# Kernel optimization log

Measured on AMD Instinct MI355X. Metric: run time of the kernel, lower is better.

Reference implementation:

```python
import jax, jax.numpy as jnp
import numpy as np

B, T, I, H, C = 16384, 1024, 1, 2, 4  # batch, seq_len, input_size, hidden_size, num_classes


def setup_inputs() -> dict:
    key = jax.random.key(0)
    ks = jax.random.split(key, 7)
    s = 1.0 / np.sqrt(H).astype(np.float32)  # PyTorch default init range
    u = lambda k, shape: jax.random.uniform(k, shape, dtype=jnp.float32, minval=-s, maxval=s)
    return {
        "x": jax.random.normal(ks[0], (B, T, I), dtype=jnp.float32),
        "W_ih": u(ks[1], (4 * H, I)),   # gate order: i, f, g, o (PyTorch convention)
        "W_hh": u(ks[2], (4 * H, H)),
        "b_ih": u(ks[3], (4 * H,)),
        "b_hh": u(ks[4], (4 * H,)),
        "W_fc": u(ks[5], (C, H)),
        "b_fc": u(ks[6], (C,)),
    }


def _lstm_last_hidden(x, W_ih, W_hh, b_ih, b_hh):
    # Precompute the input contribution for all timesteps: [B, T, 4H]
    x_proj = jnp.einsum('bti,gi->btg', x, W_ih) + (b_ih + b_hh)
    h0 = jnp.zeros((x.shape[0], H), dtype=x.dtype)
    c0 = jnp.zeros((x.shape[0], H), dtype=x.dtype)

    def step(carry, xp_t):
        h, c = carry
        gates = xp_t + h @ W_hh.T              # [B, 4H]
        i, f, g, o = jnp.split(gates, 4, axis=-1)
        c = jax.nn.sigmoid(f) * c + jax.nn.sigmoid(i) * jnp.tanh(g)
        h = jax.nn.sigmoid(o) * jnp.tanh(c)
        return (h, c), None

    (h_last, _), _ = jax.lax.scan(step, (h0, c0), jnp.swapaxes(x_proj, 0, 1))
    return h_last  # [B, H]


def reference(x, W_ih, W_hh, b_ih, b_hh, W_fc, b_fc):
    h_last = _lstm_last_hidden(x, W_ih, W_hh, b_ih, b_hh)
    return h_last @ W_fc.T + b_fc  # [B, C]
```

## Files before the change

kernel.cpp:

```cpp
#include <hip/hip_runtime.h>


typedef float f32x2 __attribute__((ext_vector_type(2)));

static __device__ __forceinline__ float fast_exp2(float x) { return __builtin_amdgcn_exp2f(x); }
static __device__ __forceinline__ float fast_rcp(float x)  { return __builtin_amdgcn_rcpf(x); }

static __device__ __forceinline__ float dpp_swap1(float v) {
    int i = __builtin_bit_cast(int, v);
    i = __builtin_amdgcn_mov_dpp(i, 0xB1, 0xF, 0xF, false);
    return __builtin_bit_cast(float, i);
}

#define SIG_SCALE  (-1.4426950408889634f)
#define TANH_SCALE ( 2.8853900817779268f)

__global__ __launch_bounds__(64, 1) void lstm_fused3(
    const float* __restrict__ x,
    const float* __restrict__ W_ih,
    const float* __restrict__ W_hh,
    const float* __restrict__ b_ih,
    const float* __restrict__ b_hh,
    const float* __restrict__ W_fc,
    const float* __restrict__ b_fc,
    float* __restrict__ out,
    int T)
{
    const int tid = blockIdx.x * 64 + threadIdx.x;
    const int e   = tid >> 1;
    const int j   = tid & 1;

    float wihs[4], whm[4], whp[4], bbs[4];
#pragma unroll
    for (int k = 0; k < 4; ++k) {
        const int g = 2 * k + j;
        const float s = (k == 2) ? TANH_SCALE : SIG_SCALE;
        wihs[k] = s * W_ih[g];
        whm[k]  = s * W_hh[2 * g + j];
        whp[k]  = s * W_hh[2 * g + (j ^ 1)];
        bbs[k]  = s * (b_ih[g] + b_hh[g]);
    }

    f32x2 wihs2[2], whm2[2], whp2[2], bbs2[2];
#pragma unroll
    for (int q = 0; q < 2; ++q) {
        wihs2[q] = f32x2{wihs[2*q], wihs[2*q+1]};
        whm2[q]  = f32x2{whm[2*q],  whm[2*q+1]};
        whp2[q]  = f32x2{whp[2*q],  whp[2*q+1]};
        bbs2[q]  = f32x2{bbs[2*q],  bbs[2*q+1]};
    }

    float hm = 0.f;
    float hp = 0.f;
    float c  = 0.f;

    const float4* xv = reinterpret_cast<const float4*>(x + (size_t)e * (size_t)T);
    const int nt4 = T >> 2;

    for (int t4 = 0; t4 < nt4; ++t4) {
        const float4 xq = xv[t4];
        const float xs[4] = {xq.x, xq.y, xq.z, xq.w};

        f32x2 xterm[4][2];
#pragma unroll
        for (int u = 0; u < 4; ++u) {
            const f32x2 xu = f32x2{xs[u], xs[u]};
#pragma unroll
            for (int q = 0; q < 2; ++q)
                xterm[u][q] = __builtin_elementwise_fma(xu, wihs2[q], bbs2[q]);
        }

#pragma unroll
        for (int u = 0; u < 4; ++u) {
            const f32x2 hmv = f32x2{hm, hm};
            const f32x2 hpv = f32x2{hp, hp};
            const f32x2 pre01 = __builtin_elementwise_fma(
                whm2[0], hmv, __builtin_elementwise_fma(whp2[0], hpv, xterm[u][0]));
            const f32x2 pre23 = __builtin_elementwise_fma(
                whm2[1], hmv, __builtin_elementwise_fma(whp2[1], hpv, xterm[u][1]));

            const float Eg = fast_exp2(pre23.x);
            const float Ef = fast_exp2(pre01.y);
            const float Ei = fast_exp2(pre01.x);
            const float Eo = fast_exp2(pre23.y);

            const float F   = 1.f + Ef;
            const float Gp  = 1.f + Eg;
            const float Ip  = 1.f + Ei;
            const float Oo  = 1.f + Eo;

            const float GmF = fmaf(Eg, F, -F);
            const float cp  = c * Ip;
            const float B   = (F * Ip) * Gp;
            const float A   = fmaf(cp, Gp, GmF);

            const float rB  = fast_rcp(B);
            c = A * rB;

            const float zc = __builtin_amdgcn_fmed3f(c, -5.f, 5.f);
            const float uu = zc * zc;
            const float p3 = fmaf(fmaf(uu + 378.f, uu, 17325.f), uu, 135135.f);
            const float q3 = fmaf(fmaf(fmaf(28.f, uu, 3150.f), uu, 62370.f), uu, 135135.f);
            const float numer = zc * p3;
            const float D     = q3 * Oo;
            const float rD    = fast_rcp(D);
            hm = numer * rD;

            hp = dpp_swap1(hm);
        }
    }

    const float h0 = j ? hp : hm;
    const float h1 = j ? hm : hp;
    const int   c0 = 2 * j;
    const float o0 = fmaf(W_fc[2*c0+0], h0, fmaf(W_fc[2*c0+1], h1, b_fc[c0]));
    const float o1 = fmaf(W_fc[2*c0+2], h0, fmaf(W_fc[2*c0+3], h1, b_fc[c0+1]));
    float2 r2; r2.x = o0; r2.y = o1;
    reinterpret_cast<float2*>(out)[e * 2 + j] = r2;
}

extern "C" void kernel_launch(void* const* d_in, const int* in_sizes, int n_in,
                              void* d_out, int out_size, void* d_ws, size_t ws_size,
                              hipStream_t stream) {
    const float* x    = (const float*)d_in[0];
    const float* W_ih = (const float*)d_in[1];
    const float* W_hh = (const float*)d_in[2];
    const float* b_ih = (const float*)d_in[3];
    const float* b_hh = (const float*)d_in[4];
    const float* W_fc = (const float*)d_in[5];
    const float* b_fc = (const float*)d_in[6];
    float* out = (float*)d_out;

    const int T = 1024;
    const int B = in_sizes[0] / T;

    dim3 block(64);
    dim3 grid((B * 2) / 64);
    lstm_fused3<<<grid, block, 0, stream>>>(x, W_ih, W_hh, b_ih, b_hh, W_fc, b_fc, out, T);
}
```

Before: 105.9 us.

## Replace exp2 gate activations with Pade tanh and carry cell state as rational pair

Computes the gate sigmoids and tanh with clamped Pade rational approximations instead of hardware exp2. The cell state is carried as an unnormalized numerator/denominator pair, rescaled by an exponent bit-trick each step, so only one reciprocal is needed per timestep. The aim is to cut transcendental-unit instructions and reciprocals from the serial recurrence and to use packed FMA on the gate polynomials. This adds many FMAs and changes accuracy, especially where clamping at ±3.5 limits the gate approximations.

```diff
diff --git a/kernel.cpp b/kernel.cpp
--- a/kernel.cpp
+++ b/kernel.cpp
@@ -3,8 +3,10 @@
 
 typedef float f32x2 __attribute__((ext_vector_type(2)));
 
-static __device__ __forceinline__ float fast_exp2(float x) { return __builtin_amdgcn_exp2f(x); }
-static __device__ __forceinline__ float fast_rcp(float x)  { return __builtin_amdgcn_rcpf(x); }
+static __device__ __forceinline__ float fast_rcp(float x) { return __builtin_amdgcn_rcpf(x); }
+static __device__ __forceinline__ float fmed3(float x, float lo, float hi) {
+    return __builtin_amdgcn_fmed3f(x, lo, hi);
+}
 
 static __device__ __forceinline__ float dpp_swap1(float v) {
     int i = __builtin_bit_cast(int, v);
@@ -12,10 +14,7 @@
     return __builtin_bit_cast(float, i);
 }
 
-#define SIG_SCALE  (-1.4426950408889634f)
-#define TANH_SCALE ( 2.8853900817779268f)
-
-__global__ __launch_bounds__(64, 1) void lstm_fused3(
+__global__ __launch_bounds__(64, 1) void lstm_fused7(
     const float* __restrict__ x,
     const float* __restrict__ W_ih,
     const float* __restrict__ W_hh,
@@ -34,7 +33,7 @@
 #pragma unroll
     for (int k = 0; k < 4; ++k) {
         const int g = 2 * k + j;
-        const float s = (k == 2) ? TANH_SCALE : SIG_SCALE;
+        const float s = (k == 2) ? 1.0f : 0.5f;
         wihs[k] = s * W_ih[g];
         whm[k]  = s * W_hh[2 * g + j];
         whp[k]  = s * W_hh[2 * g + (j ^ 1)];
@@ -50,9 +49,15 @@
         bbs2[q]  = f32x2{bbs[2*q],  bbs[2*q+1]};
     }
 
+    const f32x2 c105 = {105.f, 105.f};
+    const f32x2 c945 = {945.f, 945.f};
+    const f32x2 c15  = {15.f,  15.f};
+    const f32x2 c420 = {420.f, 420.f};
+
     float hm = 0.f;
     float hp = 0.f;
-    float c  = 0.f;
+    float Nn = 0.f;
+    float Dd = 1.f;
 
     const float4* xv = reinterpret_cast<const float4*>(x + (size_t)e * (size_t)T);
     const int nt4 = T >> 2;
@@ -79,34 +84,69 @@
             const f32x2 pre23 = __builtin_elementwise_fma(
                 whm2[1], hmv, __builtin_elementwise_fma(whp2[1], hpv, xterm[u][1]));
 
-            const float Eg = fast_exp2(pre23.x);
-            const float Ef = fast_exp2(pre01.y);
-            const float Ei = fast_exp2(pre01.x);
-            const float Eo = fast_exp2(pre23.y);
+            const f32x2 tc01 = { fmed3(pre01.x, -3.5f, 3.5f),
+                                 fmed3(pre01.y, -3.5f, 3.5f) };
+            const f32x2 tc23 = { fmed3(pre23.x, -3.5f, 3.5f),
+                                 fmed3(pre23.y, -3.5f, 3.5f) };
 
-            const float F   = 1.f + Ef;
-            const float Gp  = 1.f + Eg;
-            const float Ip  = 1.f + Ei;
-            const float Oo  = 1.f + Eo;
+            const f32x2 u01 = tc01 * tc01;
+            const f32x2 u23 = tc23 * tc23;
+            const f32x2 p01 = __builtin_elementwise_fma(u01 + c105, u01, c945);
+            const f32x2 p23 = __builtin_elementwise_fma(u23 + c105, u23, c945);
+            const f32x2 q01 = __builtin_elementwise_fma(
+                __builtin_elementwise_fma(c15, u01, c420), u01, c945);
+            const f32x2 q23 = __builtin_elementwise_fma(
+                __builtin_elementwise_fma(c15, u23, c420), u23, c945);
 
-            const float GmF = fmaf(Eg, F, -F);
-            const float cp  = c * Ip;
-            const float B   = (F * Ip) * Gp;
-            const float A   = fmaf(cp, Gp, GmF);
+            const float Sin = fmaf(tc01.x, p01.x, q01.x);
+            const float Sfn = fmaf(tc01.y, p01.y, q01.y);
+            const float Gn  = tc23.x * p23.x;
+            const float Son = fmaf(tc23.y, p23.y, q23.y);
 
-            const float rB  = fast_rcp(B);
-            c = A * rB;
+            const float cS52  = 52.5f  * Son;
+            const float cS945 = 472.5f * Son;
+            const float cShalf= 0.5f   * Son;
 
-            const float zc = __builtin_amdgcn_fmed3f(c, -5.f, 5.f);
-            const float uu = zc * zc;
-            const float p3 = fmaf(fmaf(uu + 378.f, uu, 17325.f), uu, 135135.f);
-            const float q3 = fmaf(fmaf(fmaf(28.f, uu, 3150.f), uu, 62370.f), uu, 135135.f);
-            const float numer = zc * p3;
-            const float D     = q3 * Oo;
-            const float rD    = fast_rcp(D);
-            hm = numer * rD;
+            const float QQ    = q01.x * q23.x;
+            const float SfnN  = Sfn * Nn;
+            const float T1    = SfnN * QQ;
+            const float SinGn = Sin * Gn;
+            const float qfD   = q01.y * Dd;
+            const float Nr    = fmaf(SinGn, qfD, T1);
+            const float Dr    = qfD * QQ;
+
+            const unsigned Di = __builtin_bit_cast(unsigned, Dr);
+            const float Dm = __builtin_bit_cast(float,
+                                (Di & 0x007FFFFFu) | 0x3F800000u);
+            const float sc = __builtin_bit_cast(float,
+                                0x7E800000u - (Di & 0x7F800000u));
+            const float Nm = Nr * sc;
+
+            const float B4 = 4.0f * Dm;
+            const float zN = fmed3(Nm, -B4, B4);
+            const float a  = zN * zN;
+            const float b  = Dm * Dm;
+            const float ab = a * b;
+            const float b2 = b * b;
+
+            const float t945s = cS945 * b2;
+            const float p1s   = fmaf(cS52, ab, t945s);
+            const float haS   = cShalf * a;
+            const float phs   = fmaf(haS, a, p1s);
+            const float numer = zN * phs;
+
+            const float t945b = 945.f * b2;
+            const float q1    = fmaf(420.f, ab, t945b);
+            const float a15   = 15.f * a;
+            const float qh    = fmaf(a15, a, q1);
+            const float DmQo  = Dm * q23.y;
+            const float den   = DmQo * qh;
+
+            const float r = fast_rcp(den);
+            hm = numer * r;
 
             hp = dpp_swap1(hm);
+            Nn = Nm; Dd = Dm;
         }
     }
 
@@ -136,5 +176,5 @@
 
     dim3 block(64);
     dim3 grid((B * 2) / 64);
-    lstm_fused3<<<grid, block, 0, stream>>>(x, W_ih, W_hh, b_ih, b_hh, W_fc, b_fc, out, T);
+    lstm_fused7<<<grid, block, 0, stream>>>(x, W_ih, W_hh, b_ih, b_hh, W_fc, b_fc, out, T);
 }
```

After: 145.6 us. +37.5%, slower.
